# Kernel tuning notes

Measured on AMD Instinct MI355X. Metric: run time of the kernel, lower is better.

## Reference

```python
import jax, jax.numpy as jnp
import numpy as np

B, S, D, H = 2, 2048, 1024, 16
HD = D // H
EPS = 1e-5

def _ln(x, g, b):
    mu = jnp.mean(x, axis=-1, keepdims=True)
    var = jnp.var(x, axis=-1, keepdims=True)
    return (x - mu) * jax.lax.rsqrt(var + EPS) * g + b

def setup_inputs() -> dict:
    key = jax.random.key(0)
    ks = jax.random.split(key, 6)
    sc = lambda n: 1.0 / np.sqrt(n)
    return {
        "x": jax.random.normal(ks[0], (B, S, D), jnp.float32),
        "W_qkv": jax.random.normal(ks[1], (D, 3 * D), jnp.float32) * sc(D),
        "b_qkv": jnp.zeros((3 * D,), jnp.float32),
        "W_o": jax.random.normal(ks[2], (D, D), jnp.float32) * sc(D),
        "b_o": jnp.zeros((D,), jnp.float32),
        "W_fc": jax.random.normal(ks[3], (D, 4 * D), jnp.float32) * sc(D),
        "b_fc": jnp.zeros((4 * D,), jnp.float32),
        "W_pr": jax.random.normal(ks[4], (4 * D, D), jnp.float32) * sc(4 * D),
        "b_pr": jnp.zeros((D,), jnp.float32),
        "g1": jnp.ones((D,), jnp.float32),
        "beta1": jnp.zeros((D,), jnp.float32),
        "g2": jnp.ones((D,), jnp.float32),
        "beta2": jnp.zeros((D,), jnp.float32),
    }

def reference(x, W_qkv, b_qkv, W_o, b_o, W_fc, b_fc, W_pr, b_pr, g1, beta1, g2, beta2):
    # pre-norm attention
    h = _ln(x, g1, beta1)
    qkv = h @ W_qkv + b_qkv                      # [B,S,3D]
    q, k, v = jnp.split(qkv, 3, axis=-1)
    q = q.reshape(B, S, H, HD).transpose(0, 2, 1, 3)  # [B,H,S,hd]
    k = k.reshape(B, S, H, HD).transpose(0, 2, 1, 3)
    v = v.reshape(B, S, H, HD).transpose(0, 2, 1, 3)
    scores = jnp.einsum('bhqd,bhkd->bhqk', q, k) / np.sqrt(HD)
    causal = jnp.tril(jnp.ones((S, S), bool))
    scores = jnp.where(causal, scores, -jnp.inf)
    attn = jax.nn.softmax(scores, axis=-1)
    out = jnp.einsum('bhqk,bhkd->bhqd', attn, v)
    out = out.transpose(0, 2, 1, 3).reshape(B, S, D)
    x = x + out @ W_o + b_o
    # pre-norm MLP (exact erf GELU, matching torch F.gelu default)
    h2 = _ln(x, g2, beta2)
    h2 = jax.nn.gelu(h2 @ W_fc + b_fc, approximate=False)
    x = x + h2 @ W_pr + b_pr
    return x
```

## Files before the change

kernel.cpp:

```cpp
#include <hip/hip_runtime.h>
#include <cstdint>
#include <cstddef>

#define Bb 2
#define Ss 2048
#define Dd 1024
#define Hh 16

typedef __attribute__((ext_vector_type(8))) short short8;
typedef __attribute__((ext_vector_type(4))) short short4v;
typedef __attribute__((ext_vector_type(4))) float float4v;

__device__ inline short f2bf(float f) {
  unsigned u = __builtin_bit_cast(unsigned, f);
  u = (u + 0x7fffu + ((u >> 16) & 1u)) >> 16;
  return (short)u;
}

__device__ inline float bf2f(short s) {
  unsigned u = ((unsigned)(unsigned short)s) << 16;
  return __builtin_bit_cast(float, u);
}

__device__ inline void gl_lds16(const void* g, void* l) {
  __builtin_amdgcn_global_load_lds(
      (__attribute__((address_space(1))) void*)(void*)(g),
      (__attribute__((address_space(3))) void*)(l), 16, 0, 0);
}

#define MFMA(a, b, c) __builtin_amdgcn_mfma_f32_16x16x32_bf16((a), (b), (c), 0, 0, 0)

__global__ __launch_bounds__(256) void ln_kernel(const float* __restrict__ x,
                                                 const float* __restrict__ g,
                                                 const float* __restrict__ be,
                                                 short* __restrict__ out) {
  int row = blockIdx.x;
  int tid = threadIdx.x;
  const float4* xr = (const float4*)(x + (size_t)row * Dd);
  float4 v = xr[tid];
  float s = v.x + v.y + v.z + v.w;
  float q = v.x * v.x + v.y * v.y + v.z * v.z + v.w * v.w;
#pragma unroll
  for (int off = 1; off < 64; off <<= 1) {
    s += __shfl_xor(s, off);
    q += __shfl_xor(q, off);
  }
  __shared__ float as_[4], aq_[4];
  int w = tid >> 6;
  if ((tid & 63) == 0) { as_[w] = s; aq_[w] = q; }
  __syncthreads();
  s = as_[0] + as_[1] + as_[2] + as_[3];
  q = aq_[0] + aq_[1] + aq_[2] + aq_[3];
  float mu = s * (1.0f / Dd);
  float var = q * (1.0f / Dd) - mu * mu;
  float rstd = rsqrtf(var + 1e-5f);
  const float4* g4 = (const float4*)g;
  const float4* b4 = (const float4*)be;
  float4 gv = g4[tid], bv = b4[tid];
  short4v o;
  o.x = f2bf((v.x - mu) * rstd * gv.x + bv.x);
  o.y = f2bf((v.y - mu) * rstd * gv.y + bv.y);
  o.z = f2bf((v.z - mu) * rstd * gv.z + bv.z);
  o.w = f2bf((v.w - mu) * rstd * gv.w + bv.w);
  *(short4v*)(out + (size_t)row * Dd + tid * 4) = o;
}

__global__ __launch_bounds__(256) void reduce_ln_kernel(const float* __restrict__ x,
                                                        const float* __restrict__ bias,
                                                        const short* __restrict__ parts,
                                                        const float* __restrict__ g,
                                                        const float* __restrict__ be,
                                                        float* __restrict__ x1,
                                                        short* __restrict__ h2) {
  int row = blockIdx.x, tid = threadIdx.x;
  size_t base = (size_t)row * Dd + tid * 4;
  float4 v = *(const float4*)(x + base);
  float4 bv = ((const float4*)bias)[tid];
  v.x += bv.x; v.y += bv.y; v.z += bv.z; v.w += bv.w;
#pragma unroll
  for (int s = 0; s < 2; s++) {
    short4v p = *(const short4v*)(parts + (size_t)s * 4096 * Dd + base);
    v.x += bf2f(p.x); v.y += bf2f(p.y); v.z += bf2f(p.z); v.w += bf2f(p.w);
  }
  *(float4*)(x1 + base) = v;
  float s = v.x + v.y + v.z + v.w;
  float q = v.x * v.x + v.y * v.y + v.z * v.z + v.w * v.w;
#pragma unroll
  for (int off = 1; off < 64; off <<= 1) {
    s += __shfl_xor(s, off);
    q += __shfl_xor(q, off);
  }
  __shared__ float as_[4], aq_[4];
  int w = tid >> 6;
  if ((tid & 63) == 0) { as_[w] = s; aq_[w] = q; }
  __syncthreads();
  s = as_[0] + as_[1] + as_[2] + as_[3];
  q = aq_[0] + aq_[1] + aq_[2] + aq_[3];
  float mu = s * (1.0f / Dd);
  float var = q * (1.0f / Dd) - mu * mu;
  float rstd = rsqrtf(var + 1e-5f);
  float4 gv = ((const float4*)g)[tid], b2 = ((const float4*)be)[tid];
  short4v o;
  o.x = f2bf((v.x - mu) * rstd * gv.x + b2.x);
  o.y = f2bf((v.y - mu) * rstd * gv.y + b2.y);
  o.z = f2bf((v.z - mu) * rstd * gv.z + b2.z);
  o.w = f2bf((v.w - mu) * rstd * gv.w + b2.w);
  *(short4v*)(h2 + base) = o;
}

__global__ __launch_bounds__(256) void reduce_kernel(const float* __restrict__ src,
                                                     const float* __restrict__ bias,
                                                     const short* __restrict__ parts,
                                                     float* __restrict__ dst) {
  int row = blockIdx.x, tid = threadIdx.x;
  size_t base = (size_t)row * Dd + tid * 4;
  float4 v = *(const float4*)(src + base);
  float4 bv = ((const float4*)bias)[tid];
  v.x += bv.x; v.y += bv.y; v.z += bv.z; v.w += bv.w;
#pragma unroll
  for (int s = 0; s < 2; s++) {
    short4v p = *(const short4v*)(parts + (size_t)s * 4096 * Dd + base);
    v.x += bf2f(p.x); v.y += bf2f(p.y); v.z += bf2f(p.z); v.w += bf2f(p.w);
  }
  *(float4*)(dst + base) = v;
}

__global__ __launch_bounds__(256) void wt_all_kernel(const float* __restrict__ W0,
                                                     short* __restrict__ T0,
                                                     const float* __restrict__ W1,
                                                     short* __restrict__ T1,
                                                     const float* __restrict__ W2,
                                                     short* __restrict__ T2,
                                                     const float* __restrict__ W3,
                                                     short* __restrict__ T3) {
  __shared__ float t[32][33];
  int id = blockIdx.x;
  const float* W; short* Wt; int N, K, tix;
  if (id < 3072)      { W = W0; Wt = T0; N = 3072; K = 1024; tix = id; }
  else if (id < 4096) { W = W1; Wt = T1; N = 1024; K = 1024; tix = id - 3072; }
  else if (id < 8192) { W = W2; Wt = T2; N = 4096; K = 1024; tix = id - 4096; }
  else                { W = W3; Wt = T3; N = 1024; K = 4096; tix = id - 8192; }
  int nx = N / 32;
  int n0 = (tix % nx) * 32, k0 = (tix / nx) * 32;
  int tx = threadIdx.x & 31, ty = threadIdx.x >> 5;
#pragma unroll
  for (int i = 0; i < 4; i++)
    t[ty + 8 * i][tx] = W[(size_t)(k0 + ty + 8 * i) * N + n0 + tx];
  __syncthreads();
#pragma unroll
  for (int i = 0; i < 4; i++)
    Wt[(size_t)(n0 + ty + 8 * i) * K + k0 + tx] = f2bf(t[tx][ty + 8 * i]);
}

__global__ __launch_bounds__(256) void vt_kernel(const short* __restrict__ qkv,
                                                 short* __restrict__ Vt) {
  __shared__ short t[32][34];
  int s0 = blockIdx.x * 32;
  int d0 = blockIdx.y * 32;
  int bh = blockIdx.z;
  int b = bh >> 4, h = bh & 15;
  int tx = threadIdx.x & 31, ty = threadIdx.x >> 5;
#pragma unroll
  for (int i = 0; i < 4; i++)
    t[ty + 8 * i][tx] =
        qkv[(size_t)(b * Ss + s0 + ty + 8 * i) * 3072 + 2048 + h * 64 + d0 + tx];
  __syncthreads();
#pragma unroll
  for (int i = 0; i < 4; i++)
    Vt[(size_t)(bh * 64 + d0 + ty + 8 * i) * Ss + s0 + tx] = t[tx][ty + 8 * i];
}

template <int MODE>
__device__ __forceinline__ void gemm_body(const short* __restrict__ A,
                                          const short* __restrict__ Bt,
                                          const float* __restrict__ bias,
                                          void* __restrict__ outp,
                                          int M, int N, int K, int Ksplit) {
  __shared__ __align__(16) short As[128 * 64];
  __shared__ __align__(16) short Bs[128 * 64];
  const int tid = threadIdx.x;
  const int w = tid >> 6, lane = tid & 63;
  const int m0 = blockIdx.y * 128, n0 = blockIdx.x * 128;
  const int ks = blockIdx.z * Ksplit, ke = ks + Ksplit;
  const int sr = lane >> 3;
  const int sc = lane & 7;
  const int gc = sc ^ sr;
  const int fr = lane & 15;
  const int g = lane >> 4;
  const int wm = (w >> 1) * 64, wn = (w & 1) * 64;
  float4v acc[4][4] = {};
  const short* Ag = A + (size_t)(m0 + w * 32 + sr) * K + gc * 8;
  const short* Bg = Bt + (size_t)(n0 + w * 32 + sr) * K + gc * 8;
  short* Asw = As + (w * 32 + sr) * 64 + sc * 8;
  short* Bsw = Bs + (w * 32 + sr) * 64 + sc * 8;
  for (int k0 = ks; k0 < ke; k0 += 64) {
    __syncthreads();
#pragma unroll
    for (int i = 0; i < 4; i++) {
      gl_lds16(Ag + (size_t)(i * 8) * K + k0, Asw + i * 8 * 64);
      gl_lds16(Bg + (size_t)(i * 8) * K + k0, Bsw + i * 8 * 64);
    }
    __syncthreads();
#pragma unroll
    for (int kh = 0; kh < 2; kh++) {
      short8 a[4], b[4];
#pragma unroll
      for (int i = 0; i < 4; i++) {
        int row = wm + i * 16 + fr;
        int slot = (g + kh * 4) ^ (row & 7);
        a[i] = *(const short8*)(As + row * 64 + slot * 8);
      }
#pragma unroll
      for (int j = 0; j < 4; j++) {
        int row = wn + j * 16 + fr;
        int slot = (g + kh * 4) ^ (row & 7);
        b[j] = *(const short8*)(Bs + row * 64 + slot * 8);
      }
#pragma unroll
      for (int i = 0; i < 4; i++)
#pragma unroll
        for (int j = 0; j < 4; j++)
          acc[i][j] = MFMA(a[i], b[j], acc[i][j]);
    }
  }
  const int crow = g * 4;
  const int ccol = fr;
#pragma unroll
  for (int i = 0; i < 4; i++) {
#pragma unroll
    for (int j = 0; j < 4; j++) {
      int col = n0 + wn + j * 16 + ccol;
      float bcol = (MODE == 3) ? 0.f : bias[col];
#pragma unroll
      for (int r = 0; r < 4; r++) {
        int row = m0 + wm + i * 16 + crow + r;
        float v = acc[i][j][r] + bcol;
        if (MODE == 0) {
          ((short*)outp)[(size_t)row * N + col] = f2bf(v);
        } else if (MODE == 2) {
          float y = 0.79788456f * (v + 0.044715f * v * v * v);
          float e = __builtin_amdgcn_exp2f(y * 2.885390082f);
          float th = 1.0f - 2.0f * __builtin_amdgcn_rcpf(e + 1.0f);
          v = 0.5f * v * (1.0f + th);
          ((short*)outp)[(size_t)row * N + col] = f2bf(v);
        } else {
          short* pp = (short*)outp + (size_t)blockIdx.z * M * N;
          pp[(size_t)row * N + col] = f2bf(v);
        }
      }
    }
  }
}

__global__ __launch_bounds__(256) void k_gemm_qkv(const short* A, const short* Bt,
                                                  const float* bias, void* o,
                                                  int M, int N, int K, int Ks) {
  gemm_body<0>(A, Bt, bias, o, M, N, K, Ks);
}
__global__ __launch_bounds__(256) void k_gemm_fc(const short* A, const short* Bt,
                                                 const float* bias, void* o,
                                                 int M, int N, int K, int Ks) {
  gemm_body<2>(A, Bt, bias, o, M, N, K, Ks);
}
__global__ __launch_bounds__(256) void k_gemm_wo(const short* A, const short* Bt,
                                                 const float* bias, void* o,
                                                 int M, int N, int K, int Ks) {
  gemm_body<3>(A, Bt, bias, o, M, N, K, Ks);
}
__global__ __launch_bounds__(256) void k_gemm_pr(const short* A, const short* Bt,
                                                 const float* bias, void* o,
                                                 int M, int N, int K, int Ks) {
  gemm_body<3>(A, Bt, bias, o, M, N, K, Ks);
}

__global__ __launch_bounds__(256) void flash_kernel(const short* __restrict__ qkv,
                                                    const short* __restrict__ Vt,
                                                    short* __restrict__ att) {
  __shared__ __align__(16) short Ks[4096];
  __shared__ __align__(16) short Vs[4096];
  __shared__ __align__(16) short P[4][16 * 72];
  const int w = threadIdx.x >> 6, lane = threadIdx.x & 63;
  const int qb = 31 - (blockIdx.x >> 5);
  const int bh = blockIdx.x & 31;
  const int b = bh >> 4, h = bh & 15;
  const int qbase = qb * 64 + w * 16;
  const int q = lane & 15;
  const int g = lane >> 4;
  const int fk = g * 8;
  short* Pw = &P[w][0];

  const int L0 = w * 64 + lane, L1 = L0 + 256;
  const int r0 = L0 >> 3, c0 = (L0 & 7) ^ (r0 & 7);
  const int r1 = L1 >> 3, c1 = (L1 & 7) ^ (r1 & 7);
  const short* kg0 = qkv + (size_t)(b * Ss + r0) * 3072 + 1024 + h * 64 + c0 * 8;
  const short* kg1 = qkv + (size_t)(b * Ss + r1) * 3072 + 1024 + h * 64 + c1 * 8;
  const short* vg0 = Vt + (size_t)(bh * 64 + r0) * Ss + c0 * 8;
  const short* vg1 = Vt + (size_t)(bh * 64 + r1) * Ss + c1 * 8;

  short8 qf[2];
  {
    const short* qrow = qkv + (size_t)(b * Ss + qbase + q) * 3072 + h * 64;
    qf[0] = *(const short8*)(qrow + fk);
    qf[1] = *(const short8*)(qrow + 32 + fk);
  }
  float4v o[4] = {};
  float l_i = 0.f;
  const float sc = 0.125f * 1.44269504088896f;
  const int nkt = qb + 1;

  for (int kt = 0; kt < nkt; kt++) {
    const int kbase = kt * 64;
    __syncthreads();
    gl_lds16(kg0 + (size_t)kbase * 3072, Ks + L0 * 8);
    gl_lds16(kg1 + (size_t)kbase * 3072, Ks + L1 * 8);
    gl_lds16(vg0 + kbase, Vs + L0 * 8);
    gl_lds16(vg1 + kbase, Vs + L1 * 8);
    __syncthreads();

    short8 kf[4][2], vf[4][2];
#pragma unroll
    for (int t = 0; t < 4; t++) {
      const int row = 16 * t + q;
      const int sw = (g ^ (row & 7)) * 8;
      kf[t][0] = *(const short8*)(Ks + row * 64 + sw);
      kf[t][1] = *(const short8*)(Ks + row * 64 + (sw ^ 32));
      vf[t][0] = *(const short8*)(Vs + row * 64 + sw);
      vf[t][1] = *(const short8*)(Vs + row * 64 + (sw ^ 32));
    }
    float4v s[4] = {};
#pragma unroll
    for (int t = 0; t < 4; t++) {
      s[t] = MFMA(kf[t][0], qf[0], s[t]);
      s[t] = MFMA(kf[t][1], qf[1], s[t]);
    }
    const bool maskt = (kbase + 63 > qbase);
    const int qlim = qbase + q - kbase;
    float p[4][4];
    float rs = 0.f;
#pragma unroll
    for (int t = 0; t < 4; t++) {
#pragma unroll
      for (int r = 0; r < 4; r++) {
        float v = s[t][r] * sc;
        if (maskt && (16 * t + 4 * g + r > qlim)) v = -3.0e38f;
        float e = __builtin_amdgcn_exp2f(v);
        p[t][r] = e;
        rs += e;
      }
    }
    rs += __shfl_xor(rs, 16);
    rs += __shfl_xor(rs, 32);
    l_i += rs;
#pragma unroll
    for (int t = 0; t < 4; t++) {
      unsigned lo = (unsigned)(unsigned short)f2bf(p[t][0]) |
                    ((unsigned)(unsigned short)f2bf(p[t][1]) << 16);
      unsigned hi = (unsigned)(unsigned short)f2bf(p[t][2]) |
                    ((unsigned)(unsigned short)f2bf(p[t][3]) << 16);
      uint2 u; u.x = lo; u.y = hi;
      *(uint2*)(Pw + q * 72 + 16 * t + 4 * g) = u;
    }
    asm volatile("s_waitcnt lgkmcnt(0)" ::: "memory");
    short8 pb0 = *(const short8*)(Pw + q * 72 + fk);
    short8 pb1 = *(const short8*)(Pw + q * 72 + 32 + fk);
#pragma unroll
    for (int t = 0; t < 4; t++) {
      o[t] = MFMA(vf[t][0], pb0, o[t]);
      o[t] = MFMA(vf[t][1], pb1, o[t]);
    }
  }
  const float inv = 1.0f / l_i;
  const int orow = b * Ss + qbase + q;
#pragma unroll
  for (int t = 0; t < 4; t++) {
    short4v ov;
    ov.x = f2bf(o[t][0] * inv);
    ov.y = f2bf(o[t][1] * inv);
    ov.z = f2bf(o[t][2] * inv);
    ov.w = f2bf(o[t][3] * inv);
    *(short4v*)(att + (size_t)orow * Dd + h * 64 + 16 * t + 4 * g) = ov;
  }
}

extern "C" void kernel_launch(void* const* d_in, const int* in_sizes, int n_in,
                              void* d_out, int out_size, void* d_ws, size_t ws_size,
                              hipStream_t stream) {
  const float* x    = (const float*)d_in[0];
  const float* Wqkv = (const float*)d_in[1];
  const float* bqkv = (const float*)d_in[2];
  const float* Wo   = (const float*)d_in[3];
  const float* bo   = (const float*)d_in[4];
  const float* Wfc  = (const float*)d_in[5];
  const float* bfc  = (const float*)d_in[6];
  const float* Wpr  = (const float*)d_in[7];
  const float* bpr  = (const float*)d_in[8];
  const float* g1   = (const float*)d_in[9];
  const float* be1  = (const float*)d_in[10];
  const float* g2   = (const float*)d_in[11];
  const float* be2  = (const float*)d_in[12];

  char* ws = (char*)d_ws;
  const size_t MB = 1024 * 1024;
  short* h1     = (short*)(ws + 0);
  short* qkvb   = (short*)(ws + 8 * MB);
  short* partWo = (short*)(ws + 0);
  short* partPr = (short*)(ws + 0);
  short* Vt     = (short*)(ws + 32 * MB);
  short* att    = (short*)(ws + 40 * MB);
  float* x1     = (float*)(ws + 48 * MB);
  short* h2     = (short*)(ws + 64 * MB);
  short* geluo  = (short*)(ws + 72 * MB);
  short* WtQkv  = (short*)(ws + 104 * MB);
  short* WtO    = (short*)(ws + 110 * MB);
  short* WtFc   = (short*)(ws + 112 * MB);
  short* WtPr   = (short*)(ws + 120 * MB);

  wt_all_kernel<<<12288, 256, 0, stream>>>(Wqkv, WtQkv, Wo, WtO, Wfc, WtFc, Wpr, WtPr);

  ln_kernel<<<4096, 256, 0, stream>>>(x, g1, be1, h1);
  k_gemm_qkv<<<dim3(3072 / 128, 4096 / 128), 256, 0, stream>>>(
      h1, WtQkv, bqkv, qkvb, 4096, 3072, 1024, 1024);
  vt_kernel<<<dim3(64, 2, 32), 256, 0, stream>>>(qkvb, Vt);
  flash_kernel<<<1024, 256, 0, stream>>>(qkvb, Vt, att);
  k_gemm_wo<<<dim3(1024 / 128, 4096 / 128, 2), 256, 0, stream>>>(
      att, WtO, nullptr, partWo, 4096, 1024, 1024, 512);
  reduce_ln_kernel<<<4096, 256, 0, stream>>>(x, bo, partWo, g2, be2, x1, h2);
  k_gemm_fc<<<dim3(4096 / 128, 4096 / 128), 256, 0, stream>>>(
      h2, WtFc, bfc, geluo, 4096, 4096, 1024, 1024);
  k_gemm_pr<<<dim3(1024 / 128, 4096 / 128, 2), 256, 0, stream>>>(
      geluo, WtPr, nullptr, partPr, 4096, 1024, 4096, 2048);
  reduce_kernel<<<4096, 256, 0, stream>>>(x1, bpr, partPr, (float*)d_out);
}
```

Before: 350.2 us.

## Fuse post-attention stages into persistent kernel with grid barriers

```diff
diff --git a/kernel.cpp b/kernel.cpp
--- a/kernel.cpp
+++ b/kernel.cpp
@@ -6,6 +6,7 @@
 #define Ss 2048
 #define Dd 1024
 #define Hh 16
+#define NBLK 512
 
 typedef __attribute__((ext_vector_type(8))) short short8;
 typedef __attribute__((ext_vector_type(4))) short short4v;
@@ -30,11 +31,23 @@
 
 #define MFMA(a, b, c) __builtin_amdgcn_mfma_f32_16x16x32_bf16((a), (b), (c), 0, 0, 0)
 
-__global__ __launch_bounds__(256) void ln_kernel(const float* __restrict__ x,
-                                                 const float* __restrict__ g,
-                                                 const float* __restrict__ be,
-                                                 short* __restrict__ out) {
-  int row = blockIdx.x;
+__device__ inline void gridbar(unsigned* bar, unsigned target) {
+  __syncthreads();
+  if (threadIdx.x == 0) {
+    __threadfence();
+    __hip_atomic_fetch_add(bar, 1u, __ATOMIC_RELEASE, __HIP_MEMORY_SCOPE_AGENT);
+    while (__hip_atomic_load(bar, __ATOMIC_ACQUIRE, __HIP_MEMORY_SCOPE_AGENT) < target)
+      __builtin_amdgcn_s_sleep(16);
+    __threadfence();
+  }
+  __syncthreads();
+}
+
+__device__ __forceinline__ void ln_row(const float* __restrict__ x,
+                                       const float* __restrict__ g,
+                                       const float* __restrict__ be,
+                                       short* __restrict__ out, int row,
+                                       float* red) {
   int tid = threadIdx.x;
   const float4* xr = (const float4*)(x + (size_t)row * Dd);
   float4 v = xr[tid];
@@ -45,96 +58,37 @@
     s += __shfl_xor(s, off);
     q += __shfl_xor(q, off);
   }
-  __shared__ float as_[4], aq_[4];
   int w = tid >> 6;
-  if ((tid & 63) == 0) { as_[w] = s; aq_[w] = q; }
-  __syncthreads();
-  s = as_[0] + as_[1] + as_[2] + as_[3];
-  q = aq_[0] + aq_[1] + aq_[2] + aq_[3];
+  if ((tid & 63) == 0) { red[w] = s; red[4 + w] = q; }
+  __syncthreads();
+  s = red[0] + red[1] + red[2] + red[3];
+  q = red[4] + red[5] + red[6] + red[7];
   float mu = s * (1.0f / Dd);
   float var = q * (1.0f / Dd) - mu * mu;
   float rstd = rsqrtf(var + 1e-5f);
-  const float4* g4 = (const float4*)g;
-  const float4* b4 = (const float4*)be;
-  float4 gv = g4[tid], bv = b4[tid];
+  float4 gv = ((const float4*)g)[tid], bv = ((const float4*)be)[tid];
   short4v o;
   o.x = f2bf((v.x - mu) * rstd * gv.x + bv.x);
   o.y = f2bf((v.y - mu) * rstd * gv.y + bv.y);
   o.z = f2bf((v.z - mu) * rstd * gv.z + bv.z);
   o.w = f2bf((v.w - mu) * rstd * gv.w + bv.w);
   *(short4v*)(out + (size_t)row * Dd + tid * 4) = o;
-}
-
-__global__ __launch_bounds__(256) void reduce_ln_kernel(const float* __restrict__ x,
-                                                        const float* __restrict__ bias,
-                                                        const short* __restrict__ parts,
-                                                        const float* __restrict__ g,
-                                                        const float* __restrict__ be,
-                                                        float* __restrict__ x1,
-                                                        short* __restrict__ h2) {
-  int row = blockIdx.x, tid = threadIdx.x;
-  size_t base = (size_t)row * Dd + tid * 4;
-  float4 v = *(const float4*)(x + base);
-  float4 bv = ((const float4*)bias)[tid];
-  v.x += bv.x; v.y += bv.y; v.z += bv.z; v.w += bv.w;
-#pragma unroll
-  for (int s = 0; s < 2; s++) {
-    short4v p = *(const short4v*)(parts + (size_t)s * 4096 * Dd + base);
-    v.x += bf2f(p.x); v.y += bf2f(p.y); v.z += bf2f(p.z); v.w += bf2f(p.w);
-  }
-  *(float4*)(x1 + base) = v;
-  float s = v.x + v.y + v.z + v.w;
-  float q = v.x * v.x + v.y * v.y + v.z * v.z + v.w * v.w;
-#pragma unroll
-  for (int off = 1; off < 64; off <<= 1) {
-    s += __shfl_xor(s, off);
-    q += __shfl_xor(q, off);
-  }
-  __shared__ float as_[4], aq_[4];
-  int w = tid >> 6;
-  if ((tid & 63) == 0) { as_[w] = s; aq_[w] = q; }
-  __syncthreads();
-  s = as_[0] + as_[1] + as_[2] + as_[3];
-  q = aq_[0] + aq_[1] + aq_[2] + aq_[3];
-  float mu = s * (1.0f / Dd);
-  float var = q * (1.0f / Dd) - mu * mu;
-  float rstd = rsqrtf(var + 1e-5f);
-  float4 gv = ((const float4*)g)[tid], b2 = ((const float4*)be)[tid];
-  short4v o;
-  o.x = f2bf((v.x - mu) * rstd * gv.x + b2.x);
-  o.y = f2bf((v.y - mu) * rstd * gv.y + b2.y);
-  o.z = f2bf((v.z - mu) * rstd * gv.z + b2.z);
-  o.w = f2bf((v.w - mu) * rstd * gv.w + b2.w);
-  *(short4v*)(h2 + base) = o;
-}
-
-__global__ __launch_bounds__(256) void reduce_kernel(const float* __restrict__ src,
-                                                     const float* __restrict__ bias,
-                                                     const short* __restrict__ parts,
-                                                     float* __restrict__ dst) {
-  int row = blockIdx.x, tid = threadIdx.x;
-  size_t base = (size_t)row * Dd + tid * 4;
-  float4 v = *(const float4*)(src + base);
-  float4 bv = ((const float4*)bias)[tid];
-  v.x += bv.x; v.y += bv.y; v.z += bv.z; v.w += bv.w;
-#pragma unroll
-  for (int s = 0; s < 2; s++) {
-    short4v p = *(const short4v*)(parts + (size_t)s * 4096 * Dd + base);
-    v.x += bf2f(p.x); v.y += bf2f(p.y); v.z += bf2f(p.z); v.w += bf2f(p.w);
-  }
-  *(float4*)(dst + base) = v;
-}
-
-__global__ __launch_bounds__(256) void wt_all_kernel(const float* __restrict__ W0,
-                                                     short* __restrict__ T0,
-                                                     const float* __restrict__ W1,
-                                                     short* __restrict__ T1,
-                                                     const float* __restrict__ W2,
-                                                     short* __restrict__ T2,
-                                                     const float* __restrict__ W3,
-                                                     short* __restrict__ T3) {
-  __shared__ float t[32][33];
+  __syncthreads();
+}
+
+__global__ __launch_bounds__(256) void prep_kernel(
+    const float* __restrict__ W0, short* __restrict__ T0,
+    const float* __restrict__ W1, short* __restrict__ T1,
+    const float* __restrict__ W2, short* __restrict__ T2,
+    const float* __restrict__ W3, short* __restrict__ T3,
+    const float* __restrict__ x, const float* __restrict__ g1,
+    const float* __restrict__ be1, short* __restrict__ h1) {
+  __shared__ __align__(16) float t[32][33];
   int id = blockIdx.x;
+  if (id >= 12288) {
+    ln_row(x, g1, be1, h1, id - 12288, &t[0][0]);
+    return;
+  }
   const float* W; short* Wt; int N, K, tix;
   if (id < 3072)      { W = W0; Wt = T0; N = 3072; K = 1024; tix = id; }
   else if (id < 4096) { W = W1; Wt = T1; N = 1024; K = 1024; tix = id - 3072; }
@@ -171,17 +125,17 @@
 }
 
 template <int MODE>
-__device__ __forceinline__ void gemm_body(const short* __restrict__ A,
+__device__ __forceinline__ void gemm_tile(const short* __restrict__ A,
                                           const short* __restrict__ Bt,
                                           const float* __restrict__ bias,
                                           void* __restrict__ outp,
-                                          int M, int N, int K, int Ksplit) {
-  __shared__ __align__(16) short As[128 * 64];
-  __shared__ __align__(16) short Bs[128 * 64];
+                                          int M, int N, int K,
+                                          int m0, int n0, int zp,
+                                          int ks, int ke, char* smem) {
+  short* As = (short*)smem;
+  short* Bs = (short*)smem + 128 * 64;
   const int tid = threadIdx.x;
   const int w = tid >> 6, lane = tid & 63;
-  const int m0 = blockIdx.y * 128, n0 = blockIdx.x * 128;
-  const int ks = blockIdx.z * Ksplit, ke = ks + Ksplit;
   const int sr = lane >> 3;
   const int sc = lane & 7;
   const int gc = sc ^ sr;
@@ -244,7 +198,7 @@
           v = 0.5f * v * (1.0f + th);
           ((short*)outp)[(size_t)row * N + col] = f2bf(v);
         } else {
-          short* pp = (short*)outp + (size_t)blockIdx.z * M * N;
+          short* pp = (short*)outp + (size_t)zp * M * N;
           pp[(size_t)row * N + col] = f2bf(v);
         }
       }
@@ -252,25 +206,16 @@
   }
 }
 
-__global__ __launch_bounds__(256) void k_gemm_qkv(const short* A, const short* Bt,
-                                                  const float* bias, void* o,
-                                                  int M, int N, int K, int Ks) {
-  gemm_body<0>(A, Bt, bias, o, M, N, K, Ks);
-}
-__global__ __launch_bounds__(256) void k_gemm_fc(const short* A, const short* Bt,
-                                                 const float* bias, void* o,
-                                                 int M, int N, int K, int Ks) {
-  gemm_body<2>(A, Bt, bias, o, M, N, K, Ks);
-}
-__global__ __launch_bounds__(256) void k_gemm_wo(const short* A, const short* Bt,
-                                                 const float* bias, void* o,
-                                                 int M, int N, int K, int Ks) {
-  gemm_body<3>(A, Bt, bias, o, M, N, K, Ks);
-}
-__global__ __launch_bounds__(256) void k_gemm_pr(const short* A, const short* Bt,
-                                                 const float* bias, void* o,
-                                                 int M, int N, int K, int Ks) {
-  gemm_body<3>(A, Bt, bias, o, M, N, K, Ks);
+__global__ __launch_bounds__(256) void k_gemm_qkv(const short* __restrict__ A,
+                                                  const short* __restrict__ Bt,
+                                                  const float* __restrict__ bias,
+                                                  short* __restrict__ o) {
+  __shared__ __align__(16) char smem[32768];
+  int t = blockIdx.x;
+  int c8 = t & 7, tt = t >> 3;
+  int m0 = ((c8 >> 1) * 8 + tt / 12) * 128;
+  int n0 = ((c8 & 1) * 12 + tt % 12) * 128;
+  gemm_tile<0>(A, Bt, bias, o, 4096, 3072, 1024, m0, n0, 0, 0, 1024, smem);
 }
 
 __global__ __launch_bounds__(256) void flash_kernel(const short* __restrict__ qkv,
@@ -379,6 +324,97 @@
     ov.z = f2bf(o[t][2] * inv);
     ov.w = f2bf(o[t][3] * inv);
     *(short4v*)(att + (size_t)orow * Dd + h * 64 + 16 * t + 4 * g) = ov;
+  }
+}
+
+__global__ __launch_bounds__(256, 2) void mega2(
+    const float* __restrict__ x, const float* __restrict__ bo,
+    const float* __restrict__ g2, const float* __restrict__ be2,
+    const float* __restrict__ bfc, const float* __restrict__ bpr,
+    const short* __restrict__ att, const short* __restrict__ WtO,
+    const short* __restrict__ WtFc, const short* __restrict__ WtPr,
+    short* __restrict__ partWo, float* __restrict__ x1, short* __restrict__ h2,
+    short* __restrict__ geluo, short* __restrict__ partPr,
+    float* __restrict__ out, unsigned* __restrict__ bar) {
+  __shared__ __align__(16) char smem[32768];
+  const int c = blockIdx.x;
+  const int tid = threadIdx.x;
+
+  {
+    int z = c >> 8, rem = c & 255;
+    int c8 = rem & 7, tt = rem >> 3;
+    int m0 = (c8 * 4 + tt / 8) * 128, n0 = (tt % 8) * 128;
+    gemm_tile<3>(att, WtO, nullptr, partWo, 4096, 1024, 1024, m0, n0, z,
+                 z * 512, z * 512 + 512, smem);
+  }
+  gridbar(bar + 0, NBLK);
+
+  for (int row = c; row < 4096; row += NBLK) {
+    size_t base = (size_t)row * Dd + tid * 4;
+    float4 v = *(const float4*)(x + base);
+    float4 bv = ((const float4*)bo)[tid];
+    v.x += bv.x; v.y += bv.y; v.z += bv.z; v.w += bv.w;
+#pragma unroll
+    for (int s = 0; s < 2; s++) {
+      short4v p = *(const short4v*)(partWo + (size_t)s * 4096 * Dd + base);
+      v.x += bf2f(p.x); v.y += bf2f(p.y); v.z += bf2f(p.z); v.w += bf2f(p.w);
+    }
+    *(float4*)(x1 + base) = v;
+    float s = v.x + v.y + v.z + v.w;
+    float q = v.x * v.x + v.y * v.y + v.z * v.z + v.w * v.w;
+#pragma unroll
+    for (int off = 1; off < 64; off <<= 1) {
+      s += __shfl_xor(s, off);
+      q += __shfl_xor(q, off);
+    }
+    float* red = (float*)smem;
+    int w = tid >> 6;
+    if ((tid & 63) == 0) { red[w] = s; red[4 + w] = q; }
+    __syncthreads();
+    s = red[0] + red[1] + red[2] + red[3];
+    q = red[4] + red[5] + red[6] + red[7];
+    float mu = s * (1.0f / Dd);
+    float var = q * (1.0f / Dd) - mu * mu;
+    float rstd = rsqrtf(var + 1e-5f);
+    float4 gv = ((const float4*)g2)[tid], b2 = ((const float4*)be2)[tid];
+    short4v o;
+    o.x = f2bf((v.x - mu) * rstd * gv.x + b2.x);
+    o.y = f2bf((v.y - mu) * rstd * gv.y + b2.y);
+    o.z = f2bf((v.z - mu) * rstd * gv.z + b2.z);
+    o.w = f2bf((v.w - mu) * rstd * gv.w + b2.w);
+    *(short4v*)(h2 + base) = o;
+    __syncthreads();
+  }
+  gridbar(bar + 16, NBLK);
+
+  for (int t = c; t < 1024; t += NBLK) {
+    int c8 = t & 7, tt = t >> 3;
+    int m0 = ((c8 >> 1) * 8 + tt / 16) * 128;
+    int n0 = ((c8 & 1) * 16 + tt % 16) * 128;
+    gemm_tile<2>(h2, WtFc, bfc, geluo, 4096, 4096, 1024, m0, n0, 0, 0, 1024, smem);
+  }
+  gridbar(bar + 32, NBLK);
+
+  {
+    int z = c >> 8, rem = c & 255;
+    int c8 = rem & 7, tt = rem >> 3;
+    int m0 = (c8 * 4 + tt / 8) * 128, n0 = (tt % 8) * 128;
+    gemm_tile<3>(geluo, WtPr, nullptr, partPr, 4096, 1024, 4096, m0, n0, z,
+                 z * 2048, z * 2048 + 2048, smem);
+  }
+  gridbar(bar + 48, NBLK);
+
+  for (int row = c; row < 4096; row += NBLK) {
+    size_t base = (size_t)row * Dd + tid * 4;
+    float4 v = *(const float4*)(x1 + base);
+    float4 bv = ((const float4*)bpr)[tid];
+    v.x += bv.x; v.y += bv.y; v.z += bv.z; v.w += bv.w;
+#pragma unroll
+    for (int s = 0; s < 2; s++) {
+      short4v p = *(const short4v*)(partPr + (size_t)s * 4096 * Dd + base);
+      v.x += bf2f(p.x); v.y += bf2f(p.y); v.z += bf2f(p.z); v.w += bf2f(p.w);
+    }
+    *(float4*)(out + base) = v;
   }
 }
 
@@ -405,6 +441,7 @@
   short* qkvb   = (short*)(ws + 8 * MB);
   short* partWo = (short*)(ws + 0);
   short* partPr = (short*)(ws + 0);
+  unsigned* bar = (unsigned*)(ws + 16 * MB);
   short* Vt     = (short*)(ws + 32 * MB);
   short* att    = (short*)(ws + 40 * MB);
   float* x1     = (float*)(ws + 48 * MB);
@@ -415,19 +452,13 @@
   short* WtFc   = (short*)(ws + 112 * MB);
   short* WtPr   = (short*)(ws + 120 * MB);
 
-  wt_all_kernel<<<12288, 256, 0, stream>>>(Wqkv, WtQkv, Wo, WtO, Wfc, WtFc, Wpr, WtPr);
-
-  ln_kernel<<<4096, 256, 0, stream>>>(x, g1, be1, h1);
-  k_gemm_qkv<<<dim3(3072 / 128, 4096 / 128), 256, 0, stream>>>(
-      h1, WtQkv, bqkv, qkvb, 4096, 3072, 1024, 1024);
+  prep_kernel<<<16384, 256, 0, stream>>>(Wqkv, WtQkv, Wo, WtO, Wfc, WtFc,
+                                         Wpr, WtPr, x, g1, be1, h1);
+  k_gemm_qkv<<<768, 256, 0, stream>>>(h1, WtQkv, bqkv, qkvb);
   vt_kernel<<<dim3(64, 2, 32), 256, 0, stream>>>(qkvb, Vt);
   flash_kernel<<<1024, 256, 0, stream>>>(qkvb, Vt, att);
-  k_gemm_wo<<<dim3(1024 / 128, 4096 / 128, 2), 256, 0, stream>>>(
-      att, WtO, nullptr, partWo, 4096, 1024, 1024, 512);
-  reduce_ln_kernel<<<4096, 256, 0, stream>>>(x, bo, partWo, g2, be2, x1, h2);
-  k_gemm_fc<<<dim3(4096 / 128, 4096 / 128), 256, 0, stream>>>(
-      h2, WtFc, bfc, geluo, 4096, 4096, 1024, 1024);
-  k_gemm_pr<<<dim3(1024 / 128, 4096 / 128, 2), 256, 0, stream>>>(
-      geluo, WtPr, nullptr, partPr, 4096, 1024, 4096, 2048);
-  reduce_kernel<<<4096, 256, 0, stream>>>(x1, bpr, partPr, (float*)d_out);
-}
+  hipMemsetAsync(bar, 0, 4096, stream);
+  mega2<<<NBLK, 256, 0, stream>>>(x, bo, g2, be2, bfc, bpr, att, WtO, WtFc,
+                                  WtPr, partWo, x1, h2, geluo, partPr,
+                                  (float*)d_out, bar);
+}
```

New measurement: 643.5 us. 83.8% more time.
